# Kernel optimization log

Hardware: AMD Instinct MI355X
Metric: run time of the kernel (lower is better)

The kernel has to match this reference:

```python
import jax, jax.numpy as jnp
import numpy as np

N = 2048        # num nodes
E = 65536       # num edges
C_IN = 128      # in_channels
C = 128         # out_channels (must equal C_IN for stacked layers)
H = 8           # heads
WALK_LEN = 4
NEG_SLOPE = 0.2


def compute_mask(edge_index, n, walk_length):
    # dense adjacency with duplicate-edge summation (matches sparse_coo to_dense) + self loops
    adj = jnp.zeros((n, n), jnp.float32).at[edge_index[0], edge_index[1]].add(1.0)
    adj = adj + jnp.eye(n, dtype=jnp.float32)
    kernel = jnp.eye(n, dtype=jnp.float32)
    result = kernel
    for _ in range(walk_length):
        kernel = kernel @ adj
        result = result + kernel
    # F.normalize(p=2, dim=1)
    norm = jnp.linalg.norm(result, axis=1, keepdims=True)
    return result / jnp.maximum(norm, 1e-12)


def gkat_layer(x, edge_index, mask, lin_w, att):
    n = x.shape[0]
    xh = (x @ lin_w.T).reshape(n, H, C)              # [N,H,C]
    src, dst = edge_index[0], edge_index[1]          # x_j = xh[src], x_i = xh[dst]
    att_i = att[0, :, :C]                            # [H,C]
    att_j = att[0, :, C:]                            # [H,C]
    # cat([x_i,x_j],-1)*att summed == x_i.att_i + x_j.att_j, computed per node then gathered
    s_i = jnp.einsum('nhc,hc->nh', xh, att_i)
    s_j = jnp.einsum('nhc,hc->nh', xh, att_j)
    alpha = s_i[dst] + s_j[src]                      # [E,H]
    alpha = jnp.where(alpha >= 0, alpha, NEG_SLOPE * alpha)
    alpha = alpha * mask[src, dst][:, None]          # graph-kernel mask per edge
    alpha = jax.nn.softmax(alpha, axis=0)            # global softmax over edges (faithful to F.softmax dim=0)
    # dropout: eval mode -> identity
    msg = xh[src] * alpha[:, :, None]                # [E,H,C]
    out = jax.ops.segment_sum(msg, dst, num_segments=n)  # scatter-add aggregate
    return out.mean(axis=1)                          # head mean -> [N,C]


def setup_inputs() -> dict:
    key = jax.random.key(0)
    ks = jax.random.split(key, 8)
    x = jax.random.normal(ks[0], (N, C_IN), jnp.float32)
    edge_index = jax.random.randint(ks[1], (2, E), 0, N, jnp.int64)
    # xavier-uniform-ish init
    def xav(k, shape):
        fan_in, fan_out = shape[-1], shape[0] if len(shape) == 2 else shape[-1]
        lim = float(np.sqrt(6.0 / (fan_in + fan_out)))
        return jax.random.uniform(k, shape, jnp.float32, -lim, lim)
    lin_w0 = xav(ks[2], (H * C, C_IN))
    att0 = xav(ks[3], (1, H, 2 * C))
    lin_w1 = xav(ks[4], (H * C, C))
    att1 = xav(ks[5], (1, H, 2 * C))
    skip_w = xav(ks[6], (C, C_IN))
    skip_b = jnp.zeros((C,), jnp.float32)
    return {"x": x, "edge_index": edge_index, "lin_w0": lin_w0, "att0": att0,
            "lin_w1": lin_w1, "att1": att1, "skip_w": skip_w, "skip_b": skip_b}


def reference(x, edge_index, lin_w0, att0, lin_w1, att1, skip_w, skip_b):
    mask = compute_mask(edge_index, x.shape[0], WALK_LEN)  # identical for both layers
    x_skip = x @ skip_w.T + skip_b
    h = jax.nn.relu(gkat_layer(x, edge_index, mask, lin_w0, att0))
    h = jax.nn.relu(gkat_layer(h, edge_index, mask, lin_w1, att1))
    return h + x_skip
```

## Files before the change

### kernel.cpp

```cpp
#include <hip/hip_runtime.h>
#include <hip/hip_bf16.h>

#define NN 2048
#define EE 65536
#define HH 8
#define CC 128
#define HC 1024
#define NEG_SLOPE 0.2f

__device__ __forceinline__ unsigned fenc(float f) {
    unsigned u = __float_as_uint(f);
    return (u & 0x80000000u) ? ~u : (u | 0x80000000u);
}
__device__ __forceinline__ float fdec(unsigned e) {
    return (e & 0x80000000u) ? __uint_as_float(e ^ 0x80000000u) : __uint_as_float(~e);
}

__global__ void k_deg(const int* __restrict__ ei, int* __restrict__ deg) {
    int e = blockIdx.x * 256 + threadIdx.x;
    atomicAdd(&deg[ei[EE + e]], 1);
}

__global__ void k_scan(const int* __restrict__ deg, int* __restrict__ offs) {
    __shared__ int buf[2][NN];
    int t = threadIdx.x;
    for (int i = t; i < NN; i += 1024) buf[0][i] = deg[i];
    __syncthreads();
    int cur = 0;
    for (int off = 1; off < NN; off <<= 1) {
        for (int i = t; i < NN; i += 1024) {
            int v = buf[cur][i];
            if (i >= off) v += buf[cur][i - off];
            buf[cur ^ 1][i] = v;
        }
        __syncthreads();
        cur ^= 1;
    }
    if (t == 0) offs[0] = 0;
    for (int i = t; i < NN; i += 1024) offs[i + 1] = buf[cur][i];
}

__global__ void k_scatter(const int* __restrict__ ei, const int* __restrict__ offs,
                          int* __restrict__ cursor, int* __restrict__ elist) {
    int e = blockIdx.x * 256 + threadIdx.x;
    int d = ei[EE + e];
    int p = atomicAdd(&cursor[d], 1);
    elist[offs[d] + p] = e;
}

__global__ __launch_bounds__(256) void k_build_M(
    const int* __restrict__ offs, const int* __restrict__ elist,
    const int* __restrict__ ei, float* __restrict__ M) {
    int d = blockIdx.x, t = threadIdx.x;
    __shared__ float col[NN];
    __shared__ int s_b[256], s_l[256];
    for (int i = t; i < NN; i += 256) col[i] = 0.f;
    int beg = offs[d], end = offs[d + 1];
    for (int base = beg; base < end; base += 256) {
        int m = min(256, end - base);
        __syncthreads();
        if (t < m) {
            int s = ei[elist[base + t]];
            int b = offs[s];
            s_b[t] = b;
            s_l[t] = offs[s + 1] - b;
            atomicAdd(&col[s], 3.0f);
        }
        __syncthreads();
        for (int i = 0; i < m; i++) {
            int b = s_b[i], l = s_l[i];
            for (int j = t; j < l; j += 256) {
                int u = ei[elist[b + j]];
                atomicAdd(&col[u], 1.0f);
            }
        }
    }
    __syncthreads();
    if (t == 0) col[d] += 3.0f;
    __syncthreads();
    for (int i = t; i < NN; i += 256) M[(size_t)d * NN + i] = col[i];
}

template <int EDGE_ADD, int DIAG_ADD>
__global__ __launch_bounds__(256) void k_gather(
    const float* __restrict__ Kin, float* __restrict__ Kout,
    const int* __restrict__ offs, const int* __restrict__ elist,
    const int* __restrict__ ei) {
    int d = blockIdx.x, t = threadIdx.x;
    int row0 = blockIdx.y * 256;
    __shared__ int ssrc[256];
    __shared__ float extra[256];
    if (EDGE_ADD) extra[t] = 0.f;
    const float* Kr = Kin + row0 + t;
    float acc = Kr[(size_t)d * NN];
    int beg = offs[d], end = offs[d + 1];
    for (int base = beg; base < end; base += 256) {
        int m = min(256, end - base);
        __syncthreads();
        if (t < m) {
            int s = ei[elist[base + t]];
            ssrc[t] = s;
            if (EDGE_ADD) {
                int ls = s - row0;
                if (ls >= 0 && ls < 256) atomicAdd(&extra[ls], (float)EDGE_ADD);
            }
        }
        __syncthreads();
        int k = 0;
        for (; k + 4 <= m; k += 4) {
            float v0 = Kr[(size_t)ssrc[k + 0] * NN];
            float v1 = Kr[(size_t)ssrc[k + 1] * NN];
            float v2 = Kr[(size_t)ssrc[k + 2] * NN];
            float v3 = Kr[(size_t)ssrc[k + 3] * NN];
            acc += v0 + v1 + v2 + v3;
        }
        for (; k < m; k++) acc += Kr[(size_t)ssrc[k] * NN];
    }
    if (DIAG_ADD && (d - row0) == t) acc += (float)DIAG_ADD;
    if (EDGE_ADD) {
        __syncthreads();
        acc += extra[t];
    }
    Kout[(size_t)d * NN + row0 + t] = acc;
}

__global__ void k_norm2(const float* __restrict__ R, float* __restrict__ norm2) {
    int i = blockIdx.x * 256 + threadIdx.x;
    int j0 = blockIdx.y * 128;
    float s = 0.f;
    for (int j = j0; j < j0 + 128; j++) {
        float v = R[(size_t)j * NN + i];
        s += v * v;
    }
    atomicAdd(&norm2[i], s);
}

__global__ void k_mask(const int* __restrict__ ei, const float* __restrict__ R,
                       const float* __restrict__ norm2, float* __restrict__ mask_e) {
    int e = blockIdx.x * 256 + threadIdx.x;
    int s = ei[e], d = ei[EE + e];
    float r = R[(size_t)d * NN + s];
    float nrm = sqrtf(norm2[s]);
    mask_e[e] = r / fmaxf(nrm, 1e-12f);
}

__global__ __launch_bounds__(256) void gemm_nt(
    const float* __restrict__ A, const float* __restrict__ B,
    const float* __restrict__ bias, float* __restrict__ Cout, int Ncols) {
    __shared__ float As[64][132];
    __shared__ float Bt[128][68];
    int m0 = blockIdx.x * 64, n0 = blockIdx.y * 64;
    int t = threadIdx.x;
    for (int i = t; i < 64 * 32; i += 256) {
        int r = i >> 5, c4 = i & 31;
        float4 v = *(const float4*)(A + (size_t)(m0 + r) * 128 + c4 * 4);
        *(float4*)&As[r][c4 * 4] = v;
    }
    for (int i = t; i < 64 * 32; i += 256) {
        int r = i >> 5, c4 = i & 31;
        float4 v = *(const float4*)(B + (size_t)(n0 + r) * 128 + c4 * 4);
        Bt[c4 * 4 + 0][r] = v.x;
        Bt[c4 * 4 + 1][r] = v.y;
        Bt[c4 * 4 + 2][r] = v.z;
        Bt[c4 * 4 + 3][r] = v.w;
    }
    __syncthreads();
    int ty = t >> 4, tx = t & 15;
    float acc[4][4] = {};
    for (int k = 0; k < 128; k += 4) {
        float4 b0 = *(const float4*)&Bt[k + 0][tx * 4];
        float4 b1 = *(const float4*)&Bt[k + 1][tx * 4];
        float4 b2 = *(const float4*)&Bt[k + 2][tx * 4];
        float4 b3 = *(const float4*)&Bt[k + 3][tx * 4];
#pragma unroll
        for (int r = 0; r < 4; r++) {
            float4 a = *(const float4*)&As[ty * 4 + r][k];
            acc[r][0] += a.x * b0.x + a.y * b1.x + a.z * b2.x + a.w * b3.x;
            acc[r][1] += a.x * b0.y + a.y * b1.y + a.z * b2.y + a.w * b3.y;
            acc[r][2] += a.x * b0.z + a.y * b1.z + a.z * b2.z + a.w * b3.z;
            acc[r][3] += a.x * b0.w + a.y * b1.w + a.z * b2.w + a.w * b3.w;
        }
    }
#pragma unroll
    for (int r = 0; r < 4; r++) {
        int col = n0 + tx * 4;
        float4 o = make_float4(acc[r][0], acc[r][1], acc[r][2], acc[r][3]);
        if (bias) {
            o.x += bias[col + 0]; o.y += bias[col + 1];
            o.z += bias[col + 2]; o.w += bias[col + 3];
        }
        *(float4*)(Cout + (size_t)(m0 + ty * 4 + r) * Ncols + col) = o;
    }
}

__global__ void k_scores(const float* __restrict__ xh, const float* __restrict__ att,
                         float* __restrict__ s_i, float* __restrict__ s_j) {
    int n = blockIdx.x, t = threadIdx.x;
    int h = t >> 5, lane = t & 31;
    const float* xr = xh + (size_t)n * HC + h * CC;
    const float* at = att + h * 2 * CC;
    float ai = 0.f, aj = 0.f;
    for (int c = lane; c < CC; c += 32) {
        float xv = xr[c];
        ai += xv * at[c];
        aj += xv * at[CC + c];
    }
#pragma unroll
    for (int o = 16; o > 0; o >>= 1) {
        ai += __shfl_xor(ai, o);
        aj += __shfl_xor(aj, o);
    }
    if (lane == 0) {
        s_i[n * HH + h] = ai;
        s_j[n * HH + h] = aj;
    }
}

__global__ __launch_bounds__(256) void k_alpha_z(
    const int* __restrict__ ei, const float* __restrict__ s_i,
    const float* __restrict__ s_j, const float* __restrict__ mask_e,
    float* __restrict__ zbuf, unsigned* __restrict__ gmax) {
    int t = threadIdx.x;
    int e = blockIdx.x * 256 + t;
    int s = ei[e], d = ei[EE + e];
    float me = mask_e[e];
    float4 di0 = *(const float4*)(s_i + d * HH);
    float4 di1 = *(const float4*)(s_i + d * HH + 4);
    float4 sj0 = *(const float4*)(s_j + s * HH);
    float4 sj1 = *(const float4*)(s_j + s * HH + 4);
    float z[8] = {di0.x + sj0.x, di0.y + sj0.y, di0.z + sj0.z, di0.w + sj0.w,
                  di1.x + sj1.x, di1.y + sj1.y, di1.z + sj1.z, di1.w + sj1.w};
    __shared__ float smax[HH][256];
#pragma unroll
    for (int h = 0; h < 8; h++) {
        float v = z[h];
        v = (v >= 0.f) ? v : NEG_SLOPE * v;
        v *= me;
        zbuf[(size_t)h * EE + e] = v;
        smax[h][t] = v;
    }
    __syncthreads();
    for (int s2 = 128; s2 > 0; s2 >>= 1) {
        if (t < s2) {
#pragma unroll
            for (int h = 0; h < 8; h++)
                smax[h][t] = fmaxf(smax[h][t], smax[h][t + s2]);
        }
        __syncthreads();
    }
    if (t < 8) atomicMax(&gmax[t], fenc(smax[t][0]));
}

__global__ __launch_bounds__(256) void k_softmax_sum(
    const float* __restrict__ zbuf, const unsigned* __restrict__ gmax,
    float* __restrict__ gsum) {
    int h = blockIdx.y, t = threadIdx.x;
    float mx = fdec(gmax[h]);
    const float* z = zbuf + (size_t)h * EE + blockIdx.x * 2048;
    float s = 0.f;
#pragma unroll
    for (int i = 0; i < 8; i++) s += expf(z[t + i * 256] - mx);
    __shared__ float red[256];
    red[t] = s; __syncthreads();
    for (int s2 = 128; s2 > 0; s2 >>= 1) {
        if (t < s2) red[t] += red[t + s2];
        __syncthreads();
    }
    if (t == 0) atomicAdd(&gsum[h], red[0]);
}

__global__ void k_finalize_stats(const unsigned* __restrict__ gmax,
                                 const float* __restrict__ gsum,
                                 float* __restrict__ stats) {
    int t = threadIdx.x;
    stats[t] = fdec(gmax[t]);
    stats[HH + t] = 1.0f / gsum[t];
}

__global__ __launch_bounds__(256) void k_aggregate(
    const float* __restrict__ xh, const float* __restrict__ zbuf,
    const float* __restrict__ stats, const int* __restrict__ offs,
    const int* __restrict__ elist, const int* __restrict__ ei,
    const float* __restrict__ skip, float* __restrict__ outp, int final_layer) {
    int d = blockIdx.x, t = threadIdx.x;
    int hh = t >> 7, c = t & 127;
    __shared__ float sw[32][8];
    __shared__ int ssrc[32];
    __shared__ float combine[128];
    float acc = 0.f;
    int beg = offs[d], end = offs[d + 1];
    for (int base = beg; base < end; base += 32) {
        int m = min(32, end - base);
        __syncthreads();
        if (t < m) ssrc[t] = ei[elist[base + t]];
        if (t < m * 8) {
            int k = t >> 3, h = t & 7;
            int e = elist[base + k];
            float z = zbuf[(size_t)h * EE + e];
            sw[k][h] = expf(z - stats[h]) * stats[HH + h];
        }
        __syncthreads();
        int k = 0;
        for (; k + 2 <= m; k += 2) {
            const float* x0 = xh + (size_t)ssrc[k] * HC + c;
            const float* x1 = xh + (size_t)ssrc[k + 1] * HC + c;
            float a0 = x0[hh * 128], a1 = x0[(hh + 2) * 128];
            float a2 = x0[(hh + 4) * 128], a3 = x0[(hh + 6) * 128];
            float b0 = x1[hh * 128], b1 = x1[(hh + 2) * 128];
            float b2 = x1[(hh + 4) * 128], b3 = x1[(hh + 6) * 128];
            acc += a0 * sw[k][hh] + a1 * sw[k][hh + 2] +
                   a2 * sw[k][hh + 4] + a3 * sw[k][hh + 6] +
                   b0 * sw[k + 1][hh] + b1 * sw[k + 1][hh + 2] +
                   b2 * sw[k + 1][hh + 4] + b3 * sw[k + 1][hh + 6];
        }
        if (k < m) {
            const float* x0 = xh + (size_t)ssrc[k] * HC + c;
            acc += x0[hh * 128] * sw[k][hh] + x0[(hh + 2) * 128] * sw[k][hh + 2] +
                   x0[(hh + 4) * 128] * sw[k][hh + 4] + x0[(hh + 6) * 128] * sw[k][hh + 6];
        }
    }
    if (hh == 0) combine[c] = acc;
    __syncthreads();
    if (hh == 1) combine[c] += acc;
    __syncthreads();
    if (hh == 0) {
        float v = fmaxf(combine[c] * 0.125f, 0.f);
        if (final_layer) v += skip[(size_t)d * CC + c];
        outp[(size_t)d * CC + c] = v;
    }
}

extern "C" void kernel_launch(void* const* d_in, const int* in_sizes, int n_in,
                              void* d_out, int out_size, void* d_ws, size_t ws_size,
                              hipStream_t stream) {
    const float* x    = (const float*)d_in[0];
    const int*   ei   = (const int*)d_in[1];
    const float* w0   = (const float*)d_in[2];
    const float* att0 = (const float*)d_in[3];
    const float* w1   = (const float*)d_in[4];
    const float* att1 = (const float*)d_in[5];
    const float* skw  = (const float*)d_in[6];
    const float* skb  = (const float*)d_in[7];
    float* outp = (float*)d_out;

    char* p = (char*)d_ws;
    auto alloc = [&](size_t bytes) {
        char* r = p;
        p += (bytes + 255) & ~(size_t)255;
        return r;
    };
    float* Ka     = (float*)alloc((size_t)NN * NN * 4);
    float* Kb     = (float*)alloc((size_t)NN * NN * 4);
    float* xh     = (float*)alloc((size_t)NN * HC * 4);
    float* h1     = (float*)alloc((size_t)NN * CC * 4);
    float* xskip  = (float*)alloc((size_t)NN * CC * 4);
    float* zbuf   = (float*)alloc((size_t)HH * EE * 4);
    float* mask_e = (float*)alloc((size_t)EE * 4);
    float* s_i    = (float*)alloc((size_t)NN * HH * 4);
    float* s_j    = (float*)alloc((size_t)NN * HH * 4);
    float* norm2  = (float*)alloc((size_t)NN * 4);
    float* stats  = (float*)alloc(64);
    unsigned* gmax = (unsigned*)alloc(HH * 4);
    float* gsum   = (float*)alloc(HH * 4);
    int* deg    = (int*)alloc((size_t)NN * 4);
    int* offs   = (int*)alloc((size_t)(NN + 1) * 4);
    int* cursor = (int*)alloc((size_t)NN * 4);
    int* elist  = (int*)alloc((size_t)EE * 4);

    hipMemsetAsync(deg, 0, (size_t)NN * 4, stream);
    hipMemsetAsync(cursor, 0, (size_t)NN * 4, stream);
    hipMemsetAsync(norm2, 0, (size_t)NN * 4, stream);

    k_deg<<<EE / 256, 256, 0, stream>>>(ei, deg);
    k_scan<<<1, 1024, 0, stream>>>(deg, offs);
    k_scatter<<<EE / 256, 256, 0, stream>>>(ei, offs, cursor, elist);

    k_build_M<<<NN, 256, 0, stream>>>(offs, elist, ei, Ka);
    k_gather<0, 0><<<dim3(NN, 8), 256, 0, stream>>>(Ka, Kb, offs, elist, ei);
    k_gather<1, 2><<<dim3(NN, 8), 256, 0, stream>>>(Kb, Ka, offs, elist, ei);
    k_norm2<<<dim3(NN / 256, 16), 256, 0, stream>>>(Ka, norm2);
    k_mask<<<EE / 256, 256, 0, stream>>>(ei, Ka, norm2, mask_e);

    gemm_nt<<<dim3(32, 2), 256, 0, stream>>>(x, skw, skb, xskip, 128);

    gemm_nt<<<dim3(32, 16), 256, 0, stream>>>(x, w0, nullptr, xh, 1024);
    k_scores<<<NN, 256, 0, stream>>>(xh, att0, s_i, s_j);
    hipMemsetAsync(gmax, 0, HH * 4, stream);
    hipMemsetAsync(gsum, 0, HH * 4, stream);
    k_alpha_z<<<EE / 256, 256, 0, stream>>>(ei, s_i, s_j, mask_e, zbuf, gmax);
    k_softmax_sum<<<dim3(32, HH), 256, 0, stream>>>(zbuf, gmax, gsum);
    k_finalize_stats<<<1, HH, 0, stream>>>(gmax, gsum, stats);
    k_aggregate<<<NN, 256, 0, stream>>>(xh, zbuf, stats, offs, elist, ei, nullptr, h1, 0);

    gemm_nt<<<dim3(32, 16), 256, 0, stream>>>(h1, w1, nullptr, xh, 1024);
    k_scores<<<NN, 256, 0, stream>>>(xh, att1, s_i, s_j);
    hipMemsetAsync(gmax, 0, HH * 4, stream);
    hipMemsetAsync(gsum, 0, HH * 4, stream);
    k_alpha_z<<<EE / 256, 256, 0, stream>>>(ei, s_i, s_j, mask_e, zbuf, gmax);
    k_softmax_sum<<<dim3(32, HH), 256, 0, stream>>>(zbuf, gmax, gsum);
    k_finalize_stats<<<1, HH, 0, stream>>>(gmax, gsum, stats);
    k_aggregate<<<NN, 256, 0, stream>>>(xh, zbuf, stats, offs, elist, ei, xskip, outp, 1);
}
```

Measured before the change: 360.9 us.

## Compute walk-kernel mask rows via per-source sparse propagation in shared memory

Replaces the dense N×N walk-kernel construction (build_M plus two gather passes over 16MB matrices, then a column-norm pass) with one kernel per source node. Each block holds that node's row in shared memory, runs four sparse propagation steps over a CSC adjacency, normalizes the row, and writes mask values only for that node's outgoing edges. This removes the large dense matrix traffic and workspace, and adds a reverse CSR build with 16-bit indices. The cost is about 4×E shared-memory gathers per block across 2048 blocks, with irregular per-thread work.

```diff
diff --git a/kernel.cpp b/kernel.cpp
--- a/kernel.cpp
+++ b/kernel.cpp
@@ -16,9 +16,11 @@
     return (e & 0x80000000u) ? __uint_as_float(e ^ 0x80000000u) : __uint_as_float(~e);
 }
 
-__global__ void k_deg(const int* __restrict__ ei, int* __restrict__ deg) {
+__global__ void k_deg2(const int* __restrict__ ei, int* __restrict__ deg,
+                       int* __restrict__ deg_r) {
     int e = blockIdx.x * 256 + threadIdx.x;
     atomicAdd(&deg[ei[EE + e]], 1);
+    atomicAdd(&deg_r[ei[e]], 1);
 }
 
 __global__ void k_scan(const int* __restrict__ deg, int* __restrict__ offs) {
@@ -48,100 +50,55 @@
     elist[offs[d] + p] = e;
 }
 
-__global__ __launch_bounds__(256) void k_build_M(
-    const int* __restrict__ offs, const int* __restrict__ elist,
-    const int* __restrict__ ei, float* __restrict__ M) {
-    int d = blockIdx.x, t = threadIdx.x;
-    __shared__ float col[NN];
-    __shared__ int s_b[256], s_l[256];
-    for (int i = t; i < NN; i += 256) col[i] = 0.f;
-    int beg = offs[d], end = offs[d + 1];
-    for (int base = beg; base < end; base += 256) {
-        int m = min(256, end - base);
-        __syncthreads();
-        if (t < m) {
-            int s = ei[elist[base + t]];
-            int b = offs[s];
-            s_b[t] = b;
-            s_l[t] = offs[s + 1] - b;
-            atomicAdd(&col[s], 3.0f);
-        }
-        __syncthreads();
-        for (int i = 0; i < m; i++) {
-            int b = s_b[i], l = s_l[i];
-            for (int j = t; j < l; j += 256) {
-                int u = ei[elist[b + j]];
-                atomicAdd(&col[u], 1.0f);
-            }
-        }
-    }
-    __syncthreads();
-    if (t == 0) col[d] += 3.0f;
-    __syncthreads();
-    for (int i = t; i < NN; i += 256) M[(size_t)d * NN + i] = col[i];
-}
-
-template <int EDGE_ADD, int DIAG_ADD>
-__global__ __launch_bounds__(256) void k_gather(
-    const float* __restrict__ Kin, float* __restrict__ Kout,
-    const int* __restrict__ offs, const int* __restrict__ elist,
-    const int* __restrict__ ei) {
-    int d = blockIdx.x, t = threadIdx.x;
-    int row0 = blockIdx.y * 256;
-    __shared__ int ssrc[256];
-    __shared__ float extra[256];
-    if (EDGE_ADD) extra[t] = 0.f;
-    const float* Kr = Kin + row0 + t;
-    float acc = Kr[(size_t)d * NN];
-    int beg = offs[d], end = offs[d + 1];
-    for (int base = beg; base < end; base += 256) {
-        int m = min(256, end - base);
-        __syncthreads();
-        if (t < m) {
-            int s = ei[elist[base + t]];
-            ssrc[t] = s;
-            if (EDGE_ADD) {
-                int ls = s - row0;
-                if (ls >= 0 && ls < 256) atomicAdd(&extra[ls], (float)EDGE_ADD);
-            }
-        }
-        __syncthreads();
-        int k = 0;
-        for (; k + 4 <= m; k += 4) {
-            float v0 = Kr[(size_t)ssrc[k + 0] * NN];
-            float v1 = Kr[(size_t)ssrc[k + 1] * NN];
-            float v2 = Kr[(size_t)ssrc[k + 2] * NN];
-            float v3 = Kr[(size_t)ssrc[k + 3] * NN];
-            acc += v0 + v1 + v2 + v3;
-        }
-        for (; k < m; k++) acc += Kr[(size_t)ssrc[k] * NN];
-    }
-    if (DIAG_ADD && (d - row0) == t) acc += (float)DIAG_ADD;
-    if (EDGE_ADD) {
-        __syncthreads();
-        acc += extra[t];
-    }
-    Kout[(size_t)d * NN + row0 + t] = acc;
-}
-
-__global__ void k_norm2(const float* __restrict__ R, float* __restrict__ norm2) {
-    int i = blockIdx.x * 256 + threadIdx.x;
-    int j0 = blockIdx.y * 128;
-    float s = 0.f;
-    for (int j = j0; j < j0 + 128; j++) {
-        float v = R[(size_t)j * NN + i];
-        s += v * v;
-    }
-    atomicAdd(&norm2[i], s);
-}
-
-__global__ void k_mask(const int* __restrict__ ei, const float* __restrict__ R,
-                       const float* __restrict__ norm2, float* __restrict__ mask_e) {
+__global__ void k_scatter_r(const int* __restrict__ ei, const int* __restrict__ roffs,
+                            int* __restrict__ cursor_r, unsigned short* __restrict__ csr_dst,
+                            int* __restrict__ csr_eid) {
     int e = blockIdx.x * 256 + threadIdx.x;
     int s = ei[e], d = ei[EE + e];
-    float r = R[(size_t)d * NN + s];
-    float nrm = sqrtf(norm2[s]);
-    mask_e[e] = r / fmaxf(nrm, 1e-12f);
+    int p = atomicAdd(&cursor_r[s], 1);
+    csr_dst[roffs[s] + p] = (unsigned short)d;
+    csr_eid[roffs[s] + p] = e;
+}
+
+__global__ void k_csrc(const int* __restrict__ ei, const int* __restrict__ elist,
+                       unsigned short* __restrict__ csrc) {
+    int i = blockIdx.x * 256 + threadIdx.x;
+    csrc[i] = (unsigned short)ei[elist[i]];
+}
+
+__global__ __launch_bounds__(256) void k_mask_rows(
+    const int* __restrict__ offs, const unsigned short* __restrict__ csrc,
+    const int* __restrict__ roffs, const unsigned short* __restrict__ csr_dst,
+    const int* __restrict__ csr_eid, float* __restrict__ mask_e) {
+    int s = blockIdx.x, t = threadIdx.x;
+    __shared__ float w[2][NN];
+    __shared__ int soffs[NN + 1];
+    __shared__ float red[256];
+    for (int i = t; i < NN + 1; i += 256) soffs[i] = offs[i];
+    for (int i = t; i < NN; i += 256) w[0][i] = (i == s) ? 1.f : 0.f;
+    __syncthreads();
+    int cur = 0;
+    for (int it = 0; it < 4; it++) {
+        for (int j = t; j < NN; j += 256) {
+            float acc = w[cur][j] + ((j == s) ? 1.f : 0.f);
+            int b = soffs[j], e2 = soffs[j + 1];
+            for (int c = b; c < e2; c++) acc += w[cur][csrc[c]];
+            w[cur ^ 1][j] = acc;
+        }
+        __syncthreads();
+        cur ^= 1;
+    }
+    float ss = 0.f;
+    for (int j = t; j < NN; j += 256) { float v = w[cur][j]; ss += v * v; }
+    red[t] = ss; __syncthreads();
+    for (int o = 128; o > 0; o >>= 1) {
+        if (t < o) red[t] += red[t + o];
+        __syncthreads();
+    }
+    float rnorm = 1.0f / fmaxf(sqrtf(red[0]), 1e-12f);
+    int rb = roffs[s], re = roffs[s + 1];
+    for (int c = rb + t; c < re; c += 256)
+        mask_e[csr_eid[c]] = w[cur][csr_dst[c]] * rnorm;
 }
 
 __global__ __launch_bounds__(256) void gemm_nt(
@@ -349,8 +306,6 @@
         p += (bytes + 255) & ~(size_t)255;
         return r;
     };
-    float* Ka     = (float*)alloc((size_t)NN * NN * 4);
-    float* Kb     = (float*)alloc((size_t)NN * NN * 4);
     float* xh     = (float*)alloc((size_t)NN * HC * 4);
     float* h1     = (float*)alloc((size_t)NN * CC * 4);
     float* xskip  = (float*)alloc((size_t)NN * CC * 4);
@@ -358,28 +313,33 @@
     float* mask_e = (float*)alloc((size_t)EE * 4);
     float* s_i    = (float*)alloc((size_t)NN * HH * 4);
     float* s_j    = (float*)alloc((size_t)NN * HH * 4);
-    float* norm2  = (float*)alloc((size_t)NN * 4);
     float* stats  = (float*)alloc(64);
     unsigned* gmax = (unsigned*)alloc(HH * 4);
     float* gsum   = (float*)alloc(HH * 4);
-    int* deg    = (int*)alloc((size_t)NN * 4);
-    int* offs   = (int*)alloc((size_t)(NN + 1) * 4);
-    int* cursor = (int*)alloc((size_t)NN * 4);
-    int* elist  = (int*)alloc((size_t)EE * 4);
+    int* deg      = (int*)alloc((size_t)NN * 4);
+    int* deg_r    = (int*)alloc((size_t)NN * 4);
+    int* offs     = (int*)alloc((size_t)(NN + 1) * 4);
+    int* roffs    = (int*)alloc((size_t)(NN + 1) * 4);
+    int* cursor   = (int*)alloc((size_t)NN * 4);
+    int* cursor_r = (int*)alloc((size_t)NN * 4);
+    int* elist    = (int*)alloc((size_t)EE * 4);
+    int* csr_eid  = (int*)alloc((size_t)EE * 4);
+    unsigned short* csrc    = (unsigned short*)alloc((size_t)EE * 2);
+    unsigned short* csr_dst = (unsigned short*)alloc((size_t)EE * 2);
 
     hipMemsetAsync(deg, 0, (size_t)NN * 4, stream);
+    hipMemsetAsync(deg_r, 0, (size_t)NN * 4, stream);
     hipMemsetAsync(cursor, 0, (size_t)NN * 4, stream);
-    hipMemsetAsync(norm2, 0, (size_t)NN * 4, stream);
-
-    k_deg<<<EE / 256, 256, 0, stream>>>(ei, deg);
+    hipMemsetAsync(cursor_r, 0, (size_t)NN * 4, stream);
+
+    k_deg2<<<EE / 256, 256, 0, stream>>>(ei, deg, deg_r);
     k_scan<<<1, 1024, 0, stream>>>(deg, offs);
+    k_scan<<<1, 1024, 0, stream>>>(deg_r, roffs);
     k_scatter<<<EE / 256, 256, 0, stream>>>(ei, offs, cursor, elist);
-
-    k_build_M<<<NN, 256, 0, stream>>>(offs, elist, ei, Ka);
-    k_gather<0, 0><<<dim3(NN, 8), 256, 0, stream>>>(Ka, Kb, offs, elist, ei);
-    k_gather<1, 2><<<dim3(NN, 8), 256, 0, stream>>>(Kb, Ka, offs, elist, ei);
-    k_norm2<<<dim3(NN / 256, 16), 256, 0, stream>>>(Ka, norm2);
-    k_mask<<<EE / 256, 256, 0, stream>>>(ei, Ka, norm2, mask_e);
+    k_scatter_r<<<EE / 256, 256, 0, stream>>>(ei, roffs, cursor_r, csr_dst, csr_eid);
+    k_csrc<<<EE / 256, 256, 0, stream>>>(ei, elist, csrc);
+
+    k_mask_rows<<<NN, 256, 0, stream>>>(offs, csrc, roffs, csr_dst, csr_eid, mask_e);
 
     gemm_nt<<<dim3(32, 2), 256, 0, stream>>>(x, skw, skb, xskip, 128);
 
```

Measured after the change: 945.1 us. +161.8%, slower.
